# Kernel optimization log

Measured on AMD Instinct MI355X. Metric: run time of the kernel, lower is better.

The kernel has to match this reference:

```python
import jax, jax.numpy as jnp
import numpy as np

N_HEADS = 16
HEAD_DIM = 64
DIM = 1024
BATCH = 2
SEQ = 2048


def setup_inputs() -> dict:
    key = jax.random.key(0)
    ks = jax.random.split(key, 6)
    hd = N_HEADS * HEAD_DIM
    scale_in = 1.0 / np.sqrt(DIM)
    scale_out = 1.0 / np.sqrt(hd)
    return {
        "x": jax.random.normal(ks[0], (BATCH, SEQ, DIM), dtype=jnp.float32),
        "Wq": jax.random.normal(ks[1], (DIM, hd), dtype=jnp.float32) * scale_in,
        "Wk": jax.random.normal(ks[2], (DIM, hd), dtype=jnp.float32) * scale_in,
        "Wv": jax.random.normal(ks[3], (DIM, hd), dtype=jnp.float32) * scale_in,
        "Wo": jax.random.normal(ks[4], (hd, DIM), dtype=jnp.float32) * scale_out,
        "bo": jnp.zeros((DIM,), dtype=jnp.float32),
    }


def reference(x, Wq, Wk, Wv, Wo, bo):
    b, s, _ = x.shape
    # QKV projections (bias-free Dense), reshape to [b, s, h, d]
    q = (x @ Wq).reshape(b, s, N_HEADS, HEAD_DIM)
    k = (x @ Wk).reshape(b, s, N_HEADS, HEAD_DIM)
    v = (x @ Wv).reshape(b, s, N_HEADS, HEAD_DIM)
    # scores [b, h, i, k], softmax over last axis (keys)
    dot = jnp.einsum('bihd,bkhd->bhik', q, k)
    w = jax.nn.softmax(dot / jnp.sqrt(jnp.float32(HEAD_DIM)), axis=-1)
    # weighted sum of values -> [b, i, h, d]
    a = jnp.einsum('bhij,bjhd->bihd', w, v)
    a = a.reshape(b, s, N_HEADS * HEAD_DIM)
    return a @ Wo + bo
```

## Files before the change

### kernel.cpp

```cpp
#include <hip/hip_runtime.h>
#include <hip/hip_bf16.h>
#include <math.h>

#define NH     16
#define HDIM   64
#define SEQ    2048
#define BATCH  2
#define MTOT   (BATCH*SEQ)
#define DMODEL 1024
#define HD3    3072
#define QKW    2048

#define QSCALE 0.18033688011112043f

typedef __attribute__((ext_vector_type(8))) short  short8;
typedef __attribute__((ext_vector_type(8))) ushort ushort8;
typedef __attribute__((ext_vector_type(4))) ushort ushortx4;
typedef __attribute__((ext_vector_type(4))) float  f32x4;
typedef __attribute__((ext_vector_type(2))) unsigned int u32x2;

__device__ __forceinline__ ushort f2b(float f) {
    __hip_bfloat16 h = __float2bfloat16(f);
    return *reinterpret_cast<ushort*>(&h);
}
__device__ __forceinline__ uint cvtpk(float a, float b) {
    uint r;
    asm("v_cvt_pk_bf16_f32 %0, %1, %2" : "=v"(r) : "v"(a), "v"(b));
    return r;
}
__device__ __forceinline__ float fexp2(float x) {
    float r;
    asm("v_exp_f32 %0, %1" : "=v"(r) : "v"(x));
    return r;
}

__device__ __forceinline__ void gload_lds16(const void* g, void* l) {
    __builtin_amdgcn_global_load_lds(
        (const __attribute__((address_space(1))) unsigned int*)g,
        (__attribute__((address_space(3))) unsigned int*)l, 16, 0, 0);
}

__global__ __launch_bounds__(256) void prep_kernel(
    const float* __restrict__ x,
    const float* __restrict__ Wq, const float* __restrict__ Wk,
    const float* __restrict__ Wv, const float* __restrict__ Wo,
    ushort* __restrict__ xb, ushort* __restrict__ Wt, ushort* __restrict__ Wot)
{
    __shared__ float s[64][33];
    const int tid = threadIdx.x;
    const int bid = blockIdx.x;

    if (bid < 2048) {
        const int i = bid * 256 + tid;
        const float4* p = (const float4*)(x + (size_t)i * 8);
        const float4 v0 = p[0], v1 = p[1];
        ushort8 o;
        o[0] = f2b(v0.x); o[1] = f2b(v0.y); o[2] = f2b(v0.z); o[3] = f2b(v0.w);
        o[4] = f2b(v1.x); o[5] = f2b(v1.y); o[6] = f2b(v1.z); o[7] = f2b(v1.w);
        *(ushort8*)(xb + (size_t)i * 8) = o;
        return;
    }

    const int t   = bid - 2048;
    const int z   = t >> 9;
    const int rem = t & 511;
    const int n0  = (rem & 15) * 64;
    const int k0  = (rem >> 4) * 32;
    const float* W = (z == 0) ? Wq : (z == 1) ? Wk : (z == 2) ? Wv : Wo;
    ushort* D = (z == 3) ? Wot : Wt + (size_t)z * DMODEL * DMODEL;

    #pragma unroll
    for (int i = 0; i < 8; ++i) {
        const int idx = tid + i * 256;
        const int n = idx & 63, k = idx >> 6;
        s[n][k] = W[(size_t)(k0 + k) * DMODEL + n0 + n];
    }
    __syncthreads();
    const int n  = tid >> 2;
    const int kc = (tid & 3) * 8;
    ushort8 o;
    #pragma unroll
    for (int j = 0; j < 8; ++j) o[j] = f2b(s[n][kc + j]);
    *(ushort8*)(&D[(size_t)(n0 + n) * DMODEL + k0 + kc]) = o;
}

template <typename OT, int BN>
__global__ __launch_bounds__(256) void gemm_mfma_kernel(
    const ushort* __restrict__ A, const ushort* __restrict__ Bt,
    const float* __restrict__ bias, OT* __restrict__ C,
    ushort* __restrict__ Vt,
    int M, int N, int K, int ldc, int qcols, float qscale, int nx)
{
    constexpr int NI = BN / 32;
    __shared__ __align__(16) ushort As[128 * 32];
    __shared__ __align__(16) ushort Bs[BN * 32];

    const int tid  = threadIdx.x;
    const int lane = tid & 63;
    const int lr   = lane & 15;
    const int lg   = lane >> 4;
    const int w    = tid >> 6;
    const int wm   = w >> 1, wn = w & 1;

    const int d   = blockIdx.x;
    const int xcd = d & 7;
    const int i   = d >> 3;
    const int m0 = (xcd * 4 + i / nx) * 128;
    const int n0 = (i % nx) * BN;

    f32x4 acc[4][NI];
    #pragma unroll
    for (int mi = 0; mi < 4; ++mi)
        #pragma unroll
        for (int ni = 0; ni < NI; ++ni) acc[mi][ni] = f32x4{0.f, 0.f, 0.f, 0.f};

    for (int kt = 0; kt < K; kt += 32) {
        #pragma unroll
        for (int i2 = 0; i2 < 2; ++i2) {
            const int ch  = i2 * 256 + tid;
            const int row = ch >> 2;
            const int ccd = ch & 3;
            const int ccs = ccd ^ ((row >> 1) & 3);
            gload_lds16(&A[(size_t)(m0 + row) * K + kt + ccs * 8], &As[ch * 8]);
        }
        #pragma unroll
        for (int i2 = 0; i2 < BN / 64; ++i2) {
            const int ch  = i2 * 256 + tid;
            const int row = ch >> 2;
            const int ccd = ch & 3;
            const int ccs = ccd ^ ((row >> 1) & 3);
            gload_lds16(&Bt[(size_t)(n0 + row) * K + kt + ccs * 8], &Bs[ch * 8]);
        }
        __syncthreads();

        short8 af[4], bf[NI];
        #pragma unroll
        for (int mi = 0; mi < 4; ++mi) {
            const int row = wm * 64 + mi * 16 + lr;
            af[mi] = *(const short8*)(&As[row * 32 + (lg ^ ((row >> 1) & 3)) * 8]);
        }
        #pragma unroll
        for (int ni = 0; ni < NI; ++ni) {
            const int row = wn * (BN / 2) + ni * 16 + lr;
            bf[ni] = *(const short8*)(&Bs[row * 32 + (lg ^ ((row >> 1) & 3)) * 8]);
        }
        #pragma unroll
        for (int mi = 0; mi < 4; ++mi)
            #pragma unroll
            for (int ni = 0; ni < NI; ++ni)
                acc[mi][ni] = __builtin_amdgcn_mfma_f32_16x16x32_bf16(
                    af[mi], bf[ni], acc[mi][ni], 0, 0, 0);
        __syncthreads();
    }

    if (Vt != nullptr && n0 >= 2048) {
        #pragma unroll
        for (int mi = 0; mi < 4; ++mi) {
            const int mb = m0 + wm * 64 + mi * 16 + lg * 4;
            const int bb = mb >> 11, ss = mb & 2047;
            #pragma unroll
            for (int ni = 0; ni < NI; ++ni) {
                const int n  = n0 + wn * (BN / 2) + ni * 16 + lr - 2048;
                const int h  = n >> 6, dd = n & 63;
                ushortx4 o;
                #pragma unroll
                for (int r = 0; r < 4; ++r) o[r] = f2b(acc[mi][ni][r]);
                *(ushortx4*)(&Vt[(((size_t)bb * NH + h) * HDIM + dd) * SEQ + ss]) = o;
            }
        }
        return;
    }

    #pragma unroll
    for (int mi = 0; mi < 4; ++mi) {
        #pragma unroll
        for (int ni = 0; ni < NI; ++ni) {
            const int n = n0 + wn * (BN / 2) + ni * 16 + lr;
            const float bv = bias ? bias[n] : 0.f;
            const float sc = (n < qcols) ? qscale : 1.f;
            #pragma unroll
            for (int r = 0; r < 4; ++r) {
                const int m = m0 + wm * 64 + mi * 16 + lg * 4 + r;
                const float v = (acc[mi][ni][r] + bv) * sc;
                if constexpr (sizeof(OT) == 2)
                    C[(size_t)m * ldc + n] = f2b(v);
                else
                    C[(size_t)m * ldc + n] = v;
            }
        }
    }
}

__global__ __launch_bounds__(256) void flash_attn_kernel(
    const ushort* __restrict__ QK, const ushort* __restrict__ Vt,
    ushort* __restrict__ Aout)
{
    __shared__ __align__(16) char LDS[2][16384];

    const int tid  = threadIdx.x;
    const int lane = tid & 63;
    const int w    = tid >> 6;
    const int lr   = lane & 15;
    const int lg   = lane >> 4;

    const int dblk = blockIdx.x;
    const int xcd  = dblk & 7;
    const int i    = dblk >> 3;
    const int bh   = xcd * 4 + (i >> 5);
    const int qt   = i & 31;
    const int b    = bh >> 4;
    const int h    = bh & 15;
    const int q0   = qt * 64;

    const size_t qbase = ((size_t)(b * SEQ + q0 + w * 16 + lr)) * QKW + h * HDIM;
    short8 qf[2];
    qf[0] = *(const short8*)(&QK[qbase + lg * 8]);
    qf[1] = *(const short8*)(&QK[qbase + 32 + lg * 8]);

    f32x4 O[4];
    #pragma unroll
    for (int dn = 0; dn < 4; ++dn) O[dn] = f32x4{0.f, 0.f, 0.f, 0.f};
    float li = 0.f;

    const size_t kbase  = (size_t)b * SEQ * QKW + 1024 + h * HDIM;
    const size_t vtbase = ((size_t)(b * NH + h)) * HDIM * SEQ;

    const int r0   = tid >> 3;
    const int s0   = (tid & 7) ^ (r0 & 7);
    const size_t off0 = (size_t)r0 * QKW + s0 * 8;
    const size_t off1 = off0 + (size_t)32 * QKW;

    {
        const ushort* Kg = QK + kbase;
        const ushort* Vg = Vt + vtbase;
        gload_lds16(Kg + off0, &LDS[0][tid * 16]);
        gload_lds16(Kg + off1, &LDS[0][4096 + tid * 16]);
        gload_lds16(Vg + off0, &LDS[0][8192 + tid * 16]);
        gload_lds16(Vg + off1, &LDS[0][12288 + tid * 16]);
    }

    int fbase[2];
    #pragma unroll
    for (int s = 0; s < 2; ++s)
        fbase[s] = lr * 128 + (((s * 4 + lg) * 16) ^ ((lr & 7) << 4));
    int vfb[2][2];
    #pragma unroll
    for (int s = 0; s < 2; ++s)
        #pragma unroll
        for (int hh = 0; hh < 2; ++hh)
            vfb[s][hh] = lr * 128 + ((64 * s + 32 * hh + 8 * lg) ^ ((lr & 7) << 4));

    for (int kt = 0; kt < SEQ; kt += 64) {
        const int cur = (kt >> 6) & 1;
        __syncthreads();

        if (kt + 64 < SEQ) {
            const ushort* Kg = QK + kbase + (size_t)(kt + 64) * QKW;
            const ushort* Vg = Vt + vtbase + (kt + 64);
            char* Lb = &LDS[cur ^ 1][0];
            gload_lds16(Kg + off0, Lb + tid * 16);
            gload_lds16(Kg + off1, Lb + 4096 + tid * 16);
            gload_lds16(Vg + off0, Lb + 8192 + tid * 16);
            gload_lds16(Vg + off1, Lb + 12288 + tid * 16);
        }

        const char* Kb = &LDS[cur][0]    + fbase[0];
        const char* Kc = &LDS[cur][0]    + fbase[1];
        const char* Vb = &LDS[cur][8192];

        float p[4][4];
        __builtin_amdgcn_s_setprio(1);
        #pragma unroll
        for (int sub = 0; sub < 4; ++sub) {
            f32x4 acc = {0.f, 0.f, 0.f, 0.f};
            short8 kf0 = *(const short8*)(Kb + sub * 2048);
            short8 kf1 = *(const short8*)(Kc + sub * 2048);
            acc = __builtin_amdgcn_mfma_f32_16x16x32_bf16(kf0, qf[0], acc, 0, 0, 0);
            acc = __builtin_amdgcn_mfma_f32_16x16x32_bf16(kf1, qf[1], acc, 0, 0, 0);
            #pragma unroll
            for (int r = 0; r < 4; ++r) p[sub][r] = acc[r];
        }
        __builtin_amdgcn_s_setprio(0);

        #pragma unroll
        for (int sub = 0; sub < 4; ++sub)
            #pragma unroll
            for (int r = 0; r < 4; ++r) p[sub][r] = fexp2(p[sub][r]);
        {
            const float t0 = (p[0][0] + p[0][1]) + (p[0][2] + p[0][3]);
            const float t1 = (p[1][0] + p[1][1]) + (p[1][2] + p[1][3]);
            const float t2 = (p[2][0] + p[2][1]) + (p[2][2] + p[2][3]);
            const float t3 = (p[3][0] + p[3][1]) + (p[3][2] + p[3][3]);
            li += (t0 + t1) + (t2 + t3);
        }

        short8 pf[2];
        #pragma unroll
        for (int s = 0; s < 2; ++s) {
            union { short8 v; uint u[4]; } un;
            un.u[0] = cvtpk(p[2*s+0][0], p[2*s+0][1]);
            un.u[1] = cvtpk(p[2*s+0][2], p[2*s+0][3]);
            un.u[2] = cvtpk(p[2*s+1][0], p[2*s+1][1]);
            un.u[3] = cvtpk(p[2*s+1][2], p[2*s+1][3]);
            pf[s] = un.v;
        }

        __builtin_amdgcn_s_setprio(1);
        #pragma unroll
        for (int dn = 0; dn < 4; ++dn) {
            #pragma unroll
            for (int s = 0; s < 2; ++s) {
                union { short8 v; u32x2 u2[2]; } vu;
                vu.u2[0] = *(const u32x2*)(Vb + dn * 2048 + vfb[s][0]);
                vu.u2[1] = *(const u32x2*)(Vb + dn * 2048 + vfb[s][1]);
                O[dn] = __builtin_amdgcn_mfma_f32_16x16x32_bf16(vu.v, pf[s], O[dn], 0, 0, 0);
            }
        }
        __builtin_amdgcn_s_setprio(0);
    }

    float lt = li;
    lt += __shfl_xor(lt, 16);
    lt += __shfl_xor(lt, 32);
    const float inv = 1.f / lt;
    const size_t obase = ((size_t)(b * SEQ + q0 + w * 16 + lr)) * DMODEL + h * HDIM;
    #pragma unroll
    for (int dn = 0; dn < 4; ++dn) {
        ushortx4 o;
        #pragma unroll
        for (int r = 0; r < 4; ++r) o[r] = f2b(O[dn][r] * inv);
        *(ushortx4*)(&Aout[obase + dn * 16 + lg * 4]) = o;
    }
}

extern "C" void kernel_launch(void* const* d_in, const int* in_sizes, int n_in,
                              void* d_out, int out_size, void* d_ws, size_t ws_size,
                              hipStream_t stream)
{
    const float* x  = (const float*)d_in[0];
    const float* Wq = (const float*)d_in[1];
    const float* Wk = (const float*)d_in[2];
    const float* Wv = (const float*)d_in[3];
    const float* Wo = (const float*)d_in[4];
    const float* bo = (const float*)d_in[5];
    float* out = (float*)d_out;

    ushort* xb  = (ushort*)d_ws;
    ushort* Wt  = xb  + (size_t)MTOT * DMODEL;
    ushort* Wot = Wt  + (size_t)HD3  * DMODEL;
    ushort* QK  = Wot + (size_t)DMODEL * DMODEL;
    ushort* Vt  = QK  + (size_t)MTOT * QKW;
    ushort* Ab  = xb;

    dim3 blk(256);

    prep_kernel<<<dim3(4096), blk, 0, stream>>>(x, Wq, Wk, Wv, Wo, xb, Wt, Wot);

    gemm_mfma_kernel<ushort, 128><<<dim3(768), blk, 0, stream>>>(
        xb, Wt, nullptr, QK, Vt, MTOT, HD3, DMODEL, QKW, DMODEL, QSCALE, 24);

    flash_attn_kernel<<<dim3(1024), blk, 0, stream>>>(QK, Vt, Ab);

    gemm_mfma_kernel<float, 64><<<dim3(512), blk, 0, stream>>>(
        Ab, Wot, bo, out, nullptr, MTOT, DMODEL, DMODEL, DMODEL, 0, 1.f, 16);
}
```

Measured before the change: 128.7 us.

## Double-buffer GEMM LDS tiles and load V directly to registers in attention

The projection GEMM now double-buffers its A/B LDS tiles, prefetching the next K-slice while computing the current one, and drops one barrier per iteration. The flash-attention kernel stops staging V through LDS and instead has each lane load its V fragments straight from global memory into registers at the start of each key tile. This halves attention LDS use and removes LDS traffic for V. The cost is more global load latency exposed inside the loop, plus higher register pressure that could reduce occupancy.

```diff
diff --git a/kernel.cpp b/kernel.cpp
--- a/kernel.cpp
+++ b/kernel.cpp
@@ -92,8 +92,8 @@
     int M, int N, int K, int ldc, int qcols, float qscale, int nx)
 {
     constexpr int NI = BN / 32;
-    __shared__ __align__(16) ushort As[128 * 32];
-    __shared__ __align__(16) ushort Bs[BN * 32];
+    __shared__ __align__(16) ushort As[2][128 * 32];
+    __shared__ __align__(16) ushort Bs[2][BN * 32];
 
     const int tid  = threadIdx.x;
     const int lane = tid & 63;
@@ -114,35 +114,50 @@
         #pragma unroll
         for (int ni = 0; ni < NI; ++ni) acc[mi][ni] = f32x4{0.f, 0.f, 0.f, 0.f};
 
+    #pragma unroll
+    for (int i2 = 0; i2 < 2; ++i2) {
+        const int ch  = i2 * 256 + tid;
+        const int row = ch >> 2, ccd = ch & 3, ccs = ccd ^ ((row >> 1) & 3);
+        gload_lds16(&A[(size_t)(m0 + row) * K + ccs * 8], &As[0][ch * 8]);
+    }
+    #pragma unroll
+    for (int i2 = 0; i2 < BN / 64; ++i2) {
+        const int ch  = i2 * 256 + tid;
+        const int row = ch >> 2, ccd = ch & 3, ccs = ccd ^ ((row >> 1) & 3);
+        gload_lds16(&Bt[(size_t)(n0 + row) * K + ccs * 8], &Bs[0][ch * 8]);
+    }
+
     for (int kt = 0; kt < K; kt += 32) {
-        #pragma unroll
-        for (int i2 = 0; i2 < 2; ++i2) {
-            const int ch  = i2 * 256 + tid;
-            const int row = ch >> 2;
-            const int ccd = ch & 3;
-            const int ccs = ccd ^ ((row >> 1) & 3);
-            gload_lds16(&A[(size_t)(m0 + row) * K + kt + ccs * 8], &As[ch * 8]);
-        }
-        #pragma unroll
-        for (int i2 = 0; i2 < BN / 64; ++i2) {
-            const int ch  = i2 * 256 + tid;
-            const int row = ch >> 2;
-            const int ccd = ch & 3;
-            const int ccs = ccd ^ ((row >> 1) & 3);
-            gload_lds16(&Bt[(size_t)(n0 + row) * K + kt + ccs * 8], &Bs[ch * 8]);
-        }
+        const int cur = (kt >> 5) & 1;
         __syncthreads();
+
+        if (kt + 32 < K) {
+            #pragma unroll
+            for (int i2 = 0; i2 < 2; ++i2) {
+                const int ch  = i2 * 256 + tid;
+                const int row = ch >> 2, ccd = ch & 3, ccs = ccd ^ ((row >> 1) & 3);
+                gload_lds16(&A[(size_t)(m0 + row) * K + kt + 32 + ccs * 8],
+                            &As[cur ^ 1][ch * 8]);
+            }
+            #pragma unroll
+            for (int i2 = 0; i2 < BN / 64; ++i2) {
+                const int ch  = i2 * 256 + tid;
+                const int row = ch >> 2, ccd = ch & 3, ccs = ccd ^ ((row >> 1) & 3);
+                gload_lds16(&Bt[(size_t)(n0 + row) * K + kt + 32 + ccs * 8],
+                            &Bs[cur ^ 1][ch * 8]);
+            }
+        }
 
         short8 af[4], bf[NI];
         #pragma unroll
         for (int mi = 0; mi < 4; ++mi) {
             const int row = wm * 64 + mi * 16 + lr;
-            af[mi] = *(const short8*)(&As[row * 32 + (lg ^ ((row >> 1) & 3)) * 8]);
+            af[mi] = *(const short8*)(&As[cur][row * 32 + (lg ^ ((row >> 1) & 3)) * 8]);
         }
         #pragma unroll
         for (int ni = 0; ni < NI; ++ni) {
             const int row = wn * (BN / 2) + ni * 16 + lr;
-            bf[ni] = *(const short8*)(&Bs[row * 32 + (lg ^ ((row >> 1) & 3)) * 8]);
+            bf[ni] = *(const short8*)(&Bs[cur][row * 32 + (lg ^ ((row >> 1) & 3)) * 8]);
         }
         #pragma unroll
         for (int mi = 0; mi < 4; ++mi)
@@ -150,7 +165,6 @@
             for (int ni = 0; ni < NI; ++ni)
                 acc[mi][ni] = __builtin_amdgcn_mfma_f32_16x16x32_bf16(
                     af[mi], bf[ni], acc[mi][ni], 0, 0, 0);
-        __syncthreads();
     }
 
     if (Vt != nullptr && n0 >= 2048) {
@@ -195,7 +209,7 @@
     const ushort* __restrict__ QK, const ushort* __restrict__ Vt,
     ushort* __restrict__ Aout)
 {
-    __shared__ __align__(16) char LDS[2][16384];
+    __shared__ __align__(16) char LDS[2][8192];
 
     const int tid  = threadIdx.x;
     const int lane = tid & 63;
@@ -225,6 +239,11 @@
     const size_t kbase  = (size_t)b * SEQ * QKW + 1024 + h * HDIM;
     const size_t vtbase = ((size_t)(b * NH + h)) * HDIM * SEQ;
 
+    const ushort* Vp[4];
+    #pragma unroll
+    for (int dn = 0; dn < 4; ++dn)
+        Vp[dn] = Vt + vtbase + (size_t)(dn * 16 + lr) * SEQ + 4 * lg;
+
     const int r0   = tid >> 3;
     const int s0   = (tid & 7) ^ (r0 & 7);
     const size_t off0 = (size_t)r0 * QKW + s0 * 8;
@@ -232,41 +251,38 @@
 
     {
         const ushort* Kg = QK + kbase;
-        const ushort* Vg = Vt + vtbase;
         gload_lds16(Kg + off0, &LDS[0][tid * 16]);
         gload_lds16(Kg + off1, &LDS[0][4096 + tid * 16]);
-        gload_lds16(Vg + off0, &LDS[0][8192 + tid * 16]);
-        gload_lds16(Vg + off1, &LDS[0][12288 + tid * 16]);
     }
 
     int fbase[2];
     #pragma unroll
     for (int s = 0; s < 2; ++s)
         fbase[s] = lr * 128 + (((s * 4 + lg) * 16) ^ ((lr & 7) << 4));
-    int vfb[2][2];
-    #pragma unroll
-    for (int s = 0; s < 2; ++s)
-        #pragma unroll
-        for (int hh = 0; hh < 2; ++hh)
-            vfb[s][hh] = lr * 128 + ((64 * s + 32 * hh + 8 * lg) ^ ((lr & 7) << 4));
 
     for (int kt = 0; kt < SEQ; kt += 64) {
         const int cur = (kt >> 6) & 1;
         __syncthreads();
 
+        u32x2 vpre[4][2][2];
+        #pragma unroll
+        for (int dn = 0; dn < 4; ++dn)
+            #pragma unroll
+            for (int s = 0; s < 2; ++s)
+                #pragma unroll
+                for (int hh = 0; hh < 2; ++hh)
+                    vpre[dn][s][hh] =
+                        *(const u32x2*)(Vp[dn] + kt + 32 * s + 16 * hh);
+
         if (kt + 64 < SEQ) {
             const ushort* Kg = QK + kbase + (size_t)(kt + 64) * QKW;
-            const ushort* Vg = Vt + vtbase + (kt + 64);
             char* Lb = &LDS[cur ^ 1][0];
             gload_lds16(Kg + off0, Lb + tid * 16);
             gload_lds16(Kg + off1, Lb + 4096 + tid * 16);
-            gload_lds16(Vg + off0, Lb + 8192 + tid * 16);
-            gload_lds16(Vg + off1, Lb + 12288 + tid * 16);
-        }
-
-        const char* Kb = &LDS[cur][0]    + fbase[0];
-        const char* Kc = &LDS[cur][0]    + fbase[1];
-        const char* Vb = &LDS[cur][8192];
+        }
+
+        const char* Kb = &LDS[cur][0] + fbase[0];
+        const char* Kc = &LDS[cur][0] + fbase[1];
 
         float p[4][4];
         __builtin_amdgcn_s_setprio(1);
@@ -311,8 +327,8 @@
             #pragma unroll
             for (int s = 0; s < 2; ++s) {
                 union { short8 v; u32x2 u2[2]; } vu;
-                vu.u2[0] = *(const u32x2*)(Vb + dn * 2048 + vfb[s][0]);
-                vu.u2[1] = *(const u32x2*)(Vb + dn * 2048 + vfb[s][1]);
+                vu.u2[0] = vpre[dn][s][0];
+                vu.u2[1] = vpre[dn][s][1];
                 O[dn] = __builtin_amdgcn_mfma_f32_16x16x32_bf16(vu.v, pf[s], O[dn], 0, 0, 0);
             }
         }
```

Measured after the change: 306.3 us. 2.38x slower.
